# Optimization experiments

Hardware: AMD Instinct MI355X
Metric: run time of the kernel (lower is better)

Reference implementation:

```python
import jax, jax.numpy as jnp
import numpy as np

B, N, M, C1, C2 = 4, 8192, 2048, 128, 256
H1, H2 = 256, 128  # mlp = [C2+C1, 256, 128]
EPS_DIST = 1e-8
EPS_BN = 1e-5
K = 3


def setup_inputs() -> dict:
    key = jax.random.key(0)
    ks = jax.random.split(key, 6)
    return {
        "unknown": jax.random.normal(ks[0], (B, N, 3), dtype=jnp.float32),
        "known": jax.random.normal(ks[1], (B, M, 3), dtype=jnp.float32),
        "unknow_feats": jax.random.normal(ks[2], (B, C1, N), dtype=jnp.float32),
        "known_feats": jax.random.normal(ks[3], (B, C2, M), dtype=jnp.float32),
        "W1": jax.random.normal(ks[4], (H1, C1 + C2), dtype=jnp.float32) * 0.05,
        "g1": jnp.ones((H1,), jnp.float32),
        "b1": jnp.zeros((H1,), jnp.float32),
        "W2": jax.random.normal(ks[5], (H2, H1), dtype=jnp.float32) * 0.05,
        "g2": jnp.ones((H2,), jnp.float32),
        "b2": jnp.zeros((H2,), jnp.float32),
    }


def _bn_relu(x, g, b):
    # training-mode BatchNorm over (batch, spatial) axes for (B, C, N) tensor
    mean = jnp.mean(x, axis=(0, 2), keepdims=True)
    var = jnp.var(x, axis=(0, 2), keepdims=True)
    y = (x - mean) * jax.lax.rsqrt(var + EPS_BN) * g[None, :, None] + b[None, :, None]
    return jax.nn.relu(y)


def reference(unknown, known, unknow_feats, known_feats, W1, g1, b1, W2, g2, b2):
    # 3-NN: squared euclidean distances (B, N, M) via expansion (avoids B,N,M,3 temp)
    d2 = (
        jnp.sum(unknown * unknown, axis=-1)[:, :, None]
        + jnp.sum(known * known, axis=-1)[:, None, :]
        - 2.0 * jnp.einsum("bnc,bmc->bnm", unknown, known)
    )
    neg_d, idx = jax.lax.top_k(-d2, K)  # smallest-K squared dists
    dist = -neg_d  # (B, N, K), squared distances (pytorch3d knn_points convention)
    recip = 1.0 / (dist + EPS_DIST)
    weight = recip / jnp.sum(recip, axis=2, keepdims=True)  # (B, N, K)

    kf = jnp.swapaxes(known_feats, 1, 2)  # (B, M, C2)
    grouped = jax.vmap(lambda f, i: f[i])(kf, idx)  # (B, N, K, C2)
    interp = jnp.einsum("bnkc,bnk->bcn", grouped, weight)  # (B, C2, N)

    x = jnp.concatenate([interp, unknow_feats], axis=1)  # (B, C2+C1, N)
    x = _bn_relu(jnp.einsum("oc,bcn->bon", W1, x), g1, b1)
    x = _bn_relu(jnp.einsum("oc,bcn->bon", W2, x), g2, b2)
    return x  # (B, H2, N)
```

## Files before the change

kernel.cpp:

```cpp
#include <hip/hip_runtime.h>
#include <hip/hip_bf16.h>
#include <cstdint>
#include <cstddef>

typedef unsigned short u16;
typedef __attribute__((ext_vector_type(8))) short bf16x8;
typedef __attribute__((ext_vector_type(4))) float f32x4;

constexpr int Bn = 4;
constexpr int Nq = 8192;
constexpr int Mk = 2048;
constexpr int C1c = 128;
constexpr int C2c = 256;
constexpr int H1c = 256;
constexpr int H2c = 128;

__device__ __forceinline__ float bf2f(u16 u) {
    union { uint32_t i; float f; } v;
    v.i = (uint32_t)u << 16;
    return v.f;
}
__device__ __forceinline__ u16 f2bf(float f) {
    const uint32_t x = __float_as_uint(f);
    return (u16)((x + 0x7FFFu + ((x >> 16) & 1u)) >> 16);
}
__device__ __forceinline__ uint32_t cvtpk(float lo, float hi) {
    uint32_t r;
    asm("v_cvt_pk_bf16_f32 %0, %1, %2" : "=v"(r) : "v"(lo), "v"(hi));
    return r;
}

__global__ __launch_bounds__(256) void knn_prep_kernel(
    const float* __restrict__ W1, const float* __restrict__ W2,
    u16* __restrict__ W1b, u16* __restrict__ W2b,
    const float* __restrict__ KF, u16* __restrict__ Ptb,
    const float* __restrict__ UF, u16* __restrict__ UFt,
    const float* __restrict__ unknown, const float* __restrict__ known,
    int* __restrict__ idx_out, float* __restrict__ w_out)
{
    __shared__ __align__(16) char smem[32768];
    const int bid = blockIdx.x;
    const int t = threadIdx.x;

    if (bid < 1024) {
        float4* kp = (float4*)smem;
        const int b = bid >> 8;
        const int n0 = (bid & 255) * 32;

        const float* kb = known + (size_t)b * Mk * 3;
        for (int i = t; i < Mk; i += 256) {
            const float x = kb[i * 3 + 0], y = kb[i * 3 + 1], z = kb[i * 3 + 2];
            kp[i] = make_float4(x, y, z, fmaf(x, x, fmaf(y, y, z * z)));
        }
        __syncthreads();

        const int q = n0 + (t >> 3);
        const int s = t & 7;
        const float* u = unknown + ((size_t)b * Nq + q) * 3;
        const float ux = u[0], uy = u[1], uz = u[2];
        const float nux = -2.0f * ux, nuy = -2.0f * uy, nuz = -2.0f * uz;
        const float uu = fmaf(ux, ux, fmaf(uy, uy, uz * uz));

        float d0 = 1e30f, d1 = 1e30f, d2 = 1e30f;
        int i0 = 0, i1 = 0, i2 = 0;

        auto ins = [&](float d, int i) {
            const bool c0 = d < d0, c1 = d < d1, c2 = d < d2;
            const float nd0 = fminf(d0, d);
            const float nd1 = __builtin_amdgcn_fmed3f(d0, d, d1);
            const float nd2 = __builtin_amdgcn_fmed3f(d1, d, d2);
            i2 = c1 ? i1 : (c2 ? i : i2);
            i1 = c0 ? i0 : (c1 ? i : i1);
            i0 = c0 ? i : i0;
            d0 = nd0; d1 = nd1; d2 = nd2;
        };

        #pragma unroll 8
        for (int it = 0; it < Mk / 8; ++it) {
            const int m = it * 8 + s;
            const float4 p = kp[m];
            const float d = fmaf(nux, p.x, fmaf(nuy, p.y, fmaf(nuz, p.z, p.w)));
            ins(d, m);
        }
        #pragma unroll
        for (int off = 1; off <= 4; off <<= 1) {
            const float e0 = __shfl_xor(d0, off), e1 = __shfl_xor(d1, off), e2 = __shfl_xor(d2, off);
            const int j0 = __shfl_xor(i0, off), j1 = __shfl_xor(i1, off), j2 = __shfl_xor(i2, off);
            ins(e0, j0);
            ins(e1, j1);
            ins(e2, j2);
        }
        if (s == 0) {
            const float f0 = d0 + uu, f1 = d1 + uu, f2 = d2 + uu;
            const float r0 = 1.0f / (f0 + 1e-8f);
            const float r1 = 1.0f / (f1 + 1e-8f);
            const float r2 = 1.0f / (f2 + 1e-8f);
            const float inv = 1.0f / (r0 + r1 + r2);
            const size_t base = ((size_t)b * Nq + q) * 3;
            idx_out[base + 0] = i0;
            idx_out[base + 1] = i1;
            idx_out[base + 2] = i2;
            w_out[base + 0] = r0 * inv;
            w_out[base + 1] = r1 * inv;
            w_out[base + 2] = r2 * inv;
        }
    } else if (bid < 1152) {
        const int cb = bid - 1024;
        const float* X = (cb < 96) ? W1 : W2;
        u16* Y = (cb < 96) ? W1b : W2b;
        const int i = ((cb < 96) ? cb : (cb - 96)) * 256 + t;
        const float4 v = *(const float4*)&X[(size_t)i * 4];
        ushort4 o;
        o.x = f2bf(v.x); o.y = f2bf(v.y); o.z = f2bf(v.z); o.w = f2bf(v.w);
        *(ushort4*)&Y[(size_t)i * 4] = o;
    } else if (bid < 1664) {
        u16* As = (u16*)smem;
        u16* Bs = (u16*)(smem + 5120);
        const int f = bid - 1152;
        const int b = f >> 7;
        const int rem = f & 127;
        const int m0 = (rem >> 2) * 64;
        const int h0 = (rem & 3) * 64;
        const float* KFb = KF + (size_t)b * C2c * Mk;
        const int l = t & 63, wv = t >> 6;
        const int wr = wv >> 1, wc = wv & 1;

        f32x4 acc[2][2];
        const f32x4 z = {0.0f, 0.0f, 0.0f, 0.0f};
        acc[0][0] = z; acc[0][1] = z; acc[1][0] = z; acc[1][1] = z;

        const int cA = t >> 3;
        const int mcA = (t & 7) * 8;
        const int hB = t >> 2;
        const int khB = (t & 3) * 8;

        for (int kt = 0; kt < 8; ++kt) {
            const int kc = kt * 32;
            {
                const float* src = &KFb[(size_t)(kc + cA) * Mk + m0 + mcA];
                const float4 v0 = *(const float4*)&src[0];
                const float4 v1 = *(const float4*)&src[4];
                As[(mcA + 0) * 40 + cA] = f2bf(v0.x);
                As[(mcA + 1) * 40 + cA] = f2bf(v0.y);
                As[(mcA + 2) * 40 + cA] = f2bf(v0.z);
                As[(mcA + 3) * 40 + cA] = f2bf(v0.w);
                As[(mcA + 4) * 40 + cA] = f2bf(v1.x);
                As[(mcA + 5) * 40 + cA] = f2bf(v1.y);
                As[(mcA + 6) * 40 + cA] = f2bf(v1.z);
                As[(mcA + 7) * 40 + cA] = f2bf(v1.w);
            }
            {
                const float* src = &W1[(size_t)(h0 + hB) * 384 + kc + khB];
                const float4 v0 = *(const float4*)&src[0];
                const float4 v1 = *(const float4*)&src[4];
                u16 o[8] = {f2bf(v0.x), f2bf(v0.y), f2bf(v0.z), f2bf(v0.w),
                            f2bf(v1.x), f2bf(v1.y), f2bf(v1.z), f2bf(v1.w)};
                *(uint4*)&Bs[hB * 40 + khB] = *(const uint4*)o;
            }
            __syncthreads();
            bf16x8 af[2], bf[2];
            #pragma unroll
            for (int ff = 0; ff < 2; ++ff) {
                af[ff] = *(const bf16x8*)&As[(wr * 32 + ff * 16 + (l & 15)) * 40 + (l >> 4) * 8];
                bf[ff] = *(const bf16x8*)&Bs[(wc * 32 + ff * 16 + (l & 15)) * 40 + (l >> 4) * 8];
            }
            #pragma unroll
            for (int i = 0; i < 2; ++i)
                #pragma unroll
                for (int j = 0; j < 2; ++j)
                    acc[i][j] = __builtin_amdgcn_mfma_f32_16x16x32_bf16(af[i], bf[j], acc[i][j], 0, 0, 0);
            __syncthreads();
        }

        u16* Pb = Ptb + (size_t)b * Mk * 256;
        const int cb = l & 15, rg = (l >> 4) * 4;
        #pragma unroll
        for (int i = 0; i < 2; ++i) {
            #pragma unroll
            for (int r = 0; r < 4; ++r) {
                const int row = m0 + wr * 32 + i * 16 + rg + r;
                #pragma unroll
                for (int j = 0; j < 2; ++j)
                    Pb[(size_t)row * 256 + h0 + wc * 32 + j * 16 + cb] = f2bf(acc[i][j][r]);
            }
        }
    } else {
        const int f = bid - 1664;
        const int b = f >> 8, rem = f & 255;
        const int m0 = (rem >> 1) * 64, c0 = (rem & 1) * 64;
        const float* X = UF + (size_t)b * C1c * Nq;
        u16* Y = UFt + (size_t)b * Nq * C1c;
        float (*T)[65] = (float(*)[65])smem;
        const int m4 = (t & 15) * 4, cr = t >> 4;
        #pragma unroll
        for (int i = 0; i < 4; ++i) {
            const float4 v = *(const float4*)&X[(size_t)(c0 + cr + i * 16) * Nq + m0 + m4];
            T[cr + i * 16][m4 + 0] = v.x;
            T[cr + i * 16][m4 + 1] = v.y;
            T[cr + i * 16][m4 + 2] = v.z;
            T[cr + i * 16][m4 + 3] = v.w;
        }
        __syncthreads();
        const int c4 = (t & 15) * 4, mr = t >> 4;
        #pragma unroll
        for (int i = 0; i < 4; ++i) {
            const int m = mr + i * 16;
            ushort4 o;
            o.x = f2bf(T[c4 + 0][m]);
            o.y = f2bf(T[c4 + 1][m]);
            o.z = f2bf(T[c4 + 2][m]);
            o.w = f2bf(T[c4 + 3][m]);
            *(ushort4*)&Y[(size_t)(m0 + m) * C1c + c0 + c4] = o;
        }
    }
}

__global__ __launch_bounds__(256) void mfma_gemm2(
    const u16* __restrict__ A,
    const u16* __restrict__ Bt,
    u16* __restrict__ Cout,
    const u16* __restrict__ Ptb,
    const int* __restrict__ idx, const float* __restrict__ wgt,
    float* __restrict__ partS, float* __restrict__ partQ)
{
    __shared__ u16 As[4096];
    __shared__ u16 Bs[4096];
    __shared__ float sS[2][128], sQ[2][128];

    const int b = blockIdx.z;
    const int m0 = blockIdx.x * 128, n0 = blockIdx.y * 128;
    const int t = threadIdx.x;
    const int l = t & 63, wv = t >> 6;
    const int wr = wv >> 1, wc = wv & 1;

    const u16* Ab = A + (size_t)b * Nq * C1c;
    const int rA0 = t >> 2, rA1 = (t + 256) >> 2;
    const int ko = (t & 3) * 8;

    f32x4 acc[4][4];
    const f32x4 z = {0.0f, 0.0f, 0.0f, 0.0f};
    #pragma unroll
    for (int i = 0; i < 4; ++i)
        #pragma unroll
        for (int j = 0; j < 4; ++j) acc[i][j] = z;

    uint4 a0 = *(const uint4*)&Ab[(size_t)(m0 + rA0) * C1c + ko];
    uint4 a1 = *(const uint4*)&Ab[(size_t)(m0 + rA1) * C1c + ko];
    uint4 b0 = *(const uint4*)&Bt[(size_t)(n0 + rA0) * 384 + ko];
    uint4 b1 = *(const uint4*)&Bt[(size_t)(n0 + rA1) * 384 + ko];

    for (int kt = 0; kt < C1c / 32; ++kt) {
        *(uint4*)&As[t * 8] = a0;
        *(uint4*)&As[(t + 256) * 8] = a1;
        *(uint4*)&Bs[t * 8] = b0;
        *(uint4*)&Bs[(t + 256) * 8] = b1;
        __syncthreads();
        if (kt + 1 < C1c / 32) {
            const int k0 = (kt + 1) * 32;
            a0 = *(const uint4*)&Ab[(size_t)(m0 + rA0) * C1c + k0 + ko];
            a1 = *(const uint4*)&Ab[(size_t)(m0 + rA1) * C1c + k0 + ko];
            b0 = *(const uint4*)&Bt[(size_t)(n0 + rA0) * 384 + k0 + ko];
            b1 = *(const uint4*)&Bt[(size_t)(n0 + rA1) * 384 + k0 + ko];
        }
        bf16x8 af[4], bf[4];
        #pragma unroll
        for (int f = 0; f < 4; ++f) {
            af[f] = *(const bf16x8*)&As[(wr * 64 + f * 16 + (l & 15)) * 32 + (l >> 4) * 8];
            bf[f] = *(const bf16x8*)&Bs[(wc * 64 + f * 16 + (l & 15)) * 32 + (l >> 4) * 8];
        }
        #pragma unroll
        for (int i = 0; i < 4; ++i)
            #pragma unroll
            for (int j = 0; j < 4; ++j)
                acc[i][j] = __builtin_amdgcn_mfma_f32_16x16x32_bf16(af[i], bf[j], acc[i][j], 0, 0, 0);
        __syncthreads();
    }

    const int cb = l & 15;
    const int rg = (l >> 4) * 4;
    float sj[4] = {0, 0, 0, 0}, qj[4] = {0, 0, 0, 0};
    #pragma unroll
    for (int i = 0; i < 4; ++i) {
        #pragma unroll
        for (int r = 0; r < 4; ++r) {
            const int R = m0 + wr * 64 + i * 16 + rg + r;
            const size_t ib = ((size_t)b * Nq + R) * 3;
            const int j0 = idx[ib], j1 = idx[ib + 1], j2 = idx[ib + 2];
            const float w0 = wgt[ib], w1 = wgt[ib + 1], w2 = wgt[ib + 2];
            const u16* Pb = Ptb + (size_t)b * Mk * 256;
            const u16* P0 = Pb + (size_t)j0 * 256;
            const u16* P1 = Pb + (size_t)j1 * 256;
            const u16* P2 = Pb + (size_t)j2 * 256;
            #pragma unroll
            for (int j = 0; j < 4; ++j) {
                const int Cc = n0 + wc * 64 + j * 16 + cb;
                float v = acc[i][j][r];
                v += w0 * bf2f(P0[Cc]) + w1 * bf2f(P1[Cc]) + w2 * bf2f(P2[Cc]);
                Cout[(size_t)b * Nq * 256 + (size_t)R * 256 + Cc] = f2bf(v);
                sj[j] += v;
                qj[j] += v * v;
            }
        }
    }

    #pragma unroll
    for (int j = 0; j < 4; ++j) {
        float s = sj[j], q = qj[j];
        s += __shfl_xor(s, 16); s += __shfl_xor(s, 32);
        q += __shfl_xor(q, 16); q += __shfl_xor(q, 32);
        if (l < 16) {
            sS[wr][wc * 64 + j * 16 + l] = s;
            sQ[wr][wc * 64 + j * 16 + l] = q;
        }
    }
    __syncthreads();
    if (t < 128) {
        const float S = sS[0][t] + sS[1][t];
        const float Q = sQ[0][t] + sQ[1][t];
        const int pblk = blockIdx.z * gridDim.x + blockIdx.x;
        partS[(size_t)pblk * 256 + blockIdx.y * 128 + t] = S;
        partQ[(size_t)pblk * 256 + blockIdx.y * 128 + t] = Q;
    }
}

__global__ __launch_bounds__(1024) void bn_finalize(
    const float* __restrict__ pS, const float* __restrict__ pQ,
    const float* __restrict__ g, const float* __restrict__ beta,
    float* __restrict__ scale, float* __restrict__ bias,
    int C, int np, float cnt)
{
    __shared__ float rs[1024], rq[1024];
    const int t = threadIdx.x;
    const int c = t & (C - 1);
    const int sl = t / C;
    const int nsl = 1024 / C;
    float s = 0.0f, q = 0.0f;
    for (int i = sl; i < np; i += nsl) {
        s += pS[(size_t)i * C + c];
        q += pQ[(size_t)i * C + c];
    }
    rs[t] = s;
    rq[t] = q;
    __syncthreads();
    if (t < C) {
        for (int k = 1; k < nsl; ++k) {
            s += rs[t + k * C];
            q += rq[t + k * C];
        }
        const float mean = s / cnt;
        const float var = q / cnt - mean * mean;
        const float r = rsqrtf(var + 1e-5f);
        const float sc = g[t] * r;
        scale[t] = sc;
        bias[t] = beta[t] - mean * sc;
    }
}

__device__ __forceinline__ uint4 bnx(uint4 x, const float* scs, const float* bis, int k) {
    const u16* p = (const u16*)&x;
    const float4 s0 = *(const float4*)&scs[k];
    const float4 s1 = *(const float4*)&scs[k + 4];
    const float4 b0 = *(const float4*)&bis[k];
    const float4 b1 = *(const float4*)&bis[k + 4];
    const float* sa = (const float*)&s0;
    const float* sb = (const float*)&s1;
    const float* ba = (const float*)&b0;
    const float* bb = (const float*)&b1;
    uint4 o;
    uint32_t* po = (uint32_t*)&o;
    #pragma unroll
    for (int w2 = 0; w2 < 2; ++w2) {
        const float a0 = fmaxf(0.0f, fmaf(bf2f(p[2 * w2 + 0]), sa[2 * w2 + 0], ba[2 * w2 + 0]));
        const float a1 = fmaxf(0.0f, fmaf(bf2f(p[2 * w2 + 1]), sa[2 * w2 + 1], ba[2 * w2 + 1]));
        po[w2] = cvtpk(a0, a1);
    }
    #pragma unroll
    for (int w2 = 0; w2 < 2; ++w2) {
        const float a0 = fmaxf(0.0f, fmaf(bf2f(p[4 + 2 * w2 + 0]), sb[2 * w2 + 0], bb[2 * w2 + 0]));
        const float a1 = fmaxf(0.0f, fmaf(bf2f(p[4 + 2 * w2 + 1]), sb[2 * w2 + 1], bb[2 * w2 + 1]));
        po[2 + w2] = cvtpk(a0, a1);
    }
    return o;
}

__global__ __launch_bounds__(256) void mfma_gemm3(
    const u16* __restrict__ W2b,
    const u16* __restrict__ Y,
    float* __restrict__ out,
    const float* __restrict__ bn_s, const float* __restrict__ bn_b,
    float* __restrict__ partS, float* __restrict__ partQ)
{
    __shared__ u16 As[2048];
    __shared__ u16 Bs[4096];
    __shared__ float scs[256], bis[256];
    __shared__ float sS[2][64], sQ[2][64];

    const int b = blockIdx.z;
    const int m0 = blockIdx.x * 64;
    const int n0 = blockIdx.y * 128;
    const int t = threadIdx.x;
    const int l = t & 63, wv = t >> 6;
    const int wr = wv >> 1, wc = wv & 1;

    scs[t] = bn_s[t];
    bis[t] = bn_b[t];

    const u16* Yb = Y + (size_t)b * Nq * 256;
    const int rA = t >> 2;
    const int rB1 = (t + 256) >> 2;
    const int ko = (t & 3) * 8;

    f32x4 acc[2][4];
    const f32x4 z = {0.0f, 0.0f, 0.0f, 0.0f};
    #pragma unroll
    for (int i = 0; i < 2; ++i)
        #pragma unroll
        for (int j = 0; j < 4; ++j) acc[i][j] = z;

    uint4 a0 = *(const uint4*)&W2b[(size_t)(m0 + rA) * 256 + ko];
    uint4 b0 = *(const uint4*)&Yb[(size_t)(n0 + rA) * 256 + ko];
    uint4 b1 = *(const uint4*)&Yb[(size_t)(n0 + rB1) * 256 + ko];
    __syncthreads();

    for (int kt = 0; kt < 8; ++kt) {
        const int k = kt * 32 + ko;
        *(uint4*)&As[t * 8] = a0;
        *(uint4*)&Bs[t * 8] = bnx(b0, scs, bis, k);
        *(uint4*)&Bs[(t + 256) * 8] = bnx(b1, scs, bis, k);
        __syncthreads();
        if (kt + 1 < 8) {
            const int k0 = (kt + 1) * 32;
            a0 = *(const uint4*)&W2b[(size_t)(m0 + rA) * 256 + k0 + ko];
            b0 = *(const uint4*)&Yb[(size_t)(n0 + rA) * 256 + k0 + ko];
            b1 = *(const uint4*)&Yb[(size_t)(n0 + rB1) * 256 + k0 + ko];
        }
        bf16x8 af[2], bf[4];
        #pragma unroll
        for (int f = 0; f < 2; ++f)
            af[f] = *(const bf16x8*)&As[(wr * 32 + f * 16 + (l & 15)) * 32 + (l >> 4) * 8];
        #pragma unroll
        for (int f = 0; f < 4; ++f)
            bf[f] = *(const bf16x8*)&Bs[(wc * 64 + f * 16 + (l & 15)) * 32 + (l >> 4) * 8];
        #pragma unroll
        for (int i = 0; i < 2; ++i)
            #pragma unroll
            for (int j = 0; j < 4; ++j)
                acc[i][j] = __builtin_amdgcn_mfma_f32_16x16x32_bf16(af[i], bf[j], acc[i][j], 0, 0, 0);
        __syncthreads();
    }

    const int cb = l & 15;
    const int rg = (l >> 4) * 4;
    float* ob = out + (size_t)b * H2c * Nq;
    #pragma unroll
    for (int i = 0; i < 2; ++i) {
        #pragma unroll
        for (int r = 0; r < 4; ++r) {
            const int Rl = wr * 32 + i * 16 + rg + r;
            #pragma unroll
            for (int j = 0; j < 4; ++j) {
                const int Cc = n0 + wc * 64 + j * 16 + cb;
                ob[(size_t)(m0 + Rl) * Nq + Cc] = acc[i][j][r];
            }
            float s = acc[i][0][r] + acc[i][1][r] + acc[i][2][r] + acc[i][3][r];
            float q = acc[i][0][r] * acc[i][0][r] + acc[i][1][r] * acc[i][1][r] +
                      acc[i][2][r] * acc[i][2][r] + acc[i][3][r] * acc[i][3][r];
            s += __shfl_xor(s, 1); s += __shfl_xor(s, 2);
            s += __shfl_xor(s, 4); s += __shfl_xor(s, 8);
            q += __shfl_xor(q, 1); q += __shfl_xor(q, 2);
            q += __shfl_xor(q, 4); q += __shfl_xor(q, 8);
            if ((l & 15) == 0) {
                sS[wc][Rl] = s;
                sQ[wc][Rl] = q;
            }
        }
    }
    __syncthreads();
    if (t < 64) {
        const float S = sS[0][t] + sS[1][t];
        const float Q = sQ[0][t] + sQ[1][t];
        const int p = blockIdx.z * gridDim.y + blockIdx.y;
        partS[(size_t)p * 128 + m0 + t] = S;
        partQ[(size_t)p * 128 + m0 + t] = Q;
    }
}

__global__ __launch_bounds__(256) void bn2_apply_kernel(
    float* __restrict__ Y,
    const float* __restrict__ pS, const float* __restrict__ pQ,
    const float* __restrict__ g, const float* __restrict__ beta)
{
    __shared__ float rs[256], rq[256];
    const int t = threadIdx.x;
    const size_t base = (size_t)blockIdx.x * 1024;
    const int c = (int)((base / Nq) % H2c);

    rs[t] = pS[(size_t)t * 128 + c];
    rq[t] = pQ[(size_t)t * 128 + c];
    __syncthreads();
    for (int off = 128; off > 0; off >>= 1) {
        if (t < off) {
            rs[t] += rs[t + off];
            rq[t] += rq[t + off];
        }
        __syncthreads();
    }
    if (t == 0) {
        const float cnt = (float)(Bn * Nq);
        const float mean = rs[0] / cnt;
        const float var = rq[0] / cnt - mean * mean;
        const float r = rsqrtf(var + 1e-5f);
        const float sc = g[c] * r;
        rs[0] = sc;
        rq[0] = beta[c] - mean * sc;
    }
    __syncthreads();
    const float sc = rs[0], bi = rq[0];
    float4 v = *(float4*)&Y[base + t * 4];
    v.x = fmaxf(0.0f, fmaf(v.x, sc, bi));
    v.y = fmaxf(0.0f, fmaf(v.y, sc, bi));
    v.z = fmaxf(0.0f, fmaf(v.z, sc, bi));
    v.w = fmaxf(0.0f, fmaf(v.w, sc, bi));
    *(float4*)&Y[base + t * 4] = v;
}

extern "C" void kernel_launch(void* const* d_in, const int* in_sizes, int n_in,
                              void* d_out, int out_size, void* d_ws, size_t ws_size,
                              hipStream_t stream) {
    const float* unknown = (const float*)d_in[0];
    const float* known = (const float*)d_in[1];
    const float* unknow_feats = (const float*)d_in[2];
    const float* known_feats = (const float*)d_in[3];
    const float* W1 = (const float*)d_in[4];
    const float* g1 = (const float*)d_in[5];
    const float* b1 = (const float*)d_in[6];
    const float* W2 = (const float*)d_in[7];
    const float* g2 = (const float*)d_in[8];
    const float* b2 = (const float*)d_in[9];
    float* out = (float*)d_out;

    char* w = (char*)d_ws;
    u16* UFt = (u16*)w; w += (size_t)Bn * Nq * C1c * 2;
    u16* W1b = (u16*)w; w += (size_t)H1c * 384 * 2;
    u16* W2b = (u16*)w; w += (size_t)H2c * H1c * 2;
    u16* Ptb = (u16*)w; w += (size_t)Bn * Mk * H1c * 2;
    u16* y1b = (u16*)w; w += (size_t)Bn * Nq * H1c * 2;
    int* idx = (int*)w; w += (size_t)Bn * Nq * 3 * 4;
    float* wgt = (float*)w; w += (size_t)Bn * Nq * 3 * 4;
    float* pS1 = (float*)w; w += (size_t)256 * 256 * 4;
    float* pQ1 = (float*)w; w += (size_t)256 * 256 * 4;
    float* pS2 = (float*)w; w += (size_t)256 * 128 * 4;
    float* pQ2 = (float*)w; w += (size_t)256 * 128 * 4;
    float* scale1 = (float*)w; w += 1024;
    float* bias1 = (float*)w; w += 1024;

    knn_prep_kernel<<<2688, 256, 0, stream>>>(W1, W2, W1b, W2b,
                                              known_feats, Ptb, unknow_feats, UFt,
                                              unknown, known, idx, wgt);

    mfma_gemm2<<<dim3(Nq / 128, H1c / 128, Bn), 256, 0, stream>>>(
        UFt, W1b + C2c, y1b, Ptb, idx, wgt, pS1, pQ1);

    bn_finalize<<<1, 1024, 0, stream>>>(pS1, pQ1, g1, b1, scale1, bias1,
                                        H1c, 256, (float)(Bn * Nq));

    mfma_gemm3<<<dim3(2, Nq / 128, Bn), 256, 0, stream>>>(
        W2b, y1b, out, scale1, bias1, pS2, pQ2);

    bn2_apply_kernel<<<(Bn * H2c * Nq) / 1024, 256, 0, stream>>>(out, pS2, pQ2, g2, b2);
}
```

Baseline: 103.4 us.

## Stage GEMM1 epilogue through LDS for vectorized gather and stores; multi-block BN finalize

The GEMM1 epilogue now writes accumulator tiles to shared memory in 32-row chunks, then each thread handles 8 contiguous channels per row. It gathers the three neighbor feature rows with 16-byte loads and writes bf16 output with 16-byte stores, replacing scattered 2-byte gathers and stores. The BN1 finalize moves from one 1024-thread block to 16 blocks of 256 threads, one per 16-channel group. The epilogue gains extra syncthreads and LDS round trips in exchange for coalesced global access.

```diff
diff --git a/kernel.cpp b/kernel.cpp
--- a/kernel.cpp
+++ b/kernel.cpp
@@ -223,9 +223,11 @@
     const int* __restrict__ idx, const float* __restrict__ wgt,
     float* __restrict__ partS, float* __restrict__ partQ)
 {
-    __shared__ u16 As[4096];
-    __shared__ u16 Bs[4096];
-    __shared__ float sS[2][128], sQ[2][128];
+    __shared__ __align__(16) char smem[16384];
+    __shared__ float redS[4][128], redQ[4][128];
+    u16* As = (u16*)smem;
+    u16* Bs = (u16*)(smem + 8192);
+    float (*Ytmp)[128] = (float(*)[128])smem;
 
     const int b = blockIdx.z;
     const int m0 = blockIdx.x * 128, n0 = blockIdx.y * 128;
@@ -278,81 +280,119 @@
 
     const int cb = l & 15;
     const int rg = (l >> 4) * 4;
-    float sj[4] = {0, 0, 0, 0}, qj[4] = {0, 0, 0, 0};
-    #pragma unroll
-    for (int i = 0; i < 4; ++i) {
-        #pragma unroll
-        for (int r = 0; r < 4; ++r) {
-            const int R = m0 + wr * 64 + i * 16 + rg + r;
+    const int colblk = t & 15;
+    const int rowblk = t >> 4;
+    float s8[8] = {0, 0, 0, 0, 0, 0, 0, 0}, q8[8] = {0, 0, 0, 0, 0, 0, 0, 0};
+    const u16* Pb = Ptb + (size_t)b * Mk * 256;
+
+    for (int q = 0; q < 4; ++q) {
+        __syncthreads();
+        if (wr == (q >> 1)) {
+            #pragma unroll
+            for (int ii = 0; ii < 2; ++ii) {
+                const int i = (q & 1) * 2 + ii;
+                #pragma unroll
+                for (int r = 0; r < 4; ++r) {
+                    const int Rq = ii * 16 + rg + r;
+                    #pragma unroll
+                    for (int j = 0; j < 4; ++j)
+                        Ytmp[Rq][wc * 64 + j * 16 + cb] = acc[i][j][r];
+                }
+            }
+        }
+        __syncthreads();
+        #pragma unroll
+        for (int rr = 0; rr < 2; ++rr) {
+            const int Rq = rowblk * 2 + rr;
+            const int R = m0 + q * 32 + Rq;
             const size_t ib = ((size_t)b * Nq + R) * 3;
             const int j0 = idx[ib], j1 = idx[ib + 1], j2 = idx[ib + 2];
             const float w0 = wgt[ib], w1 = wgt[ib + 1], w2 = wgt[ib + 2];
-            const u16* Pb = Ptb + (size_t)b * Mk * 256;
-            const u16* P0 = Pb + (size_t)j0 * 256;
-            const u16* P1 = Pb + (size_t)j1 * 256;
-            const u16* P2 = Pb + (size_t)j2 * 256;
-            #pragma unroll
-            for (int j = 0; j < 4; ++j) {
-                const int Cc = n0 + wc * 64 + j * 16 + cb;
-                float v = acc[i][j][r];
-                v += w0 * bf2f(P0[Cc]) + w1 * bf2f(P1[Cc]) + w2 * bf2f(P2[Cc]);
-                Cout[(size_t)b * Nq * 256 + (size_t)R * 256 + Cc] = f2bf(v);
-                sj[j] += v;
-                qj[j] += v * v;
-            }
+            const int c8 = colblk * 8;
+            const int Cc0 = n0 + c8;
+            const float* yrow = &Ytmp[Rq][c8];
+            const float4 y0 = *(const float4*)&yrow[0];
+            const float4 y1v = *(const float4*)&yrow[4];
+            const uint4 p0 = *(const uint4*)&Pb[(size_t)j0 * 256 + Cc0];
+            const uint4 p1 = *(const uint4*)&Pb[(size_t)j1 * 256 + Cc0];
+            const uint4 p2 = *(const uint4*)&Pb[(size_t)j2 * 256 + Cc0];
+            const u16* pp0 = (const u16*)&p0;
+            const u16* pp1 = (const u16*)&p1;
+            const u16* pp2 = (const u16*)&p2;
+            const float* ya = (const float*)&y0;
+            const float* yb = (const float*)&y1v;
+            float v[8];
+            #pragma unroll
+            for (int c = 0; c < 8; ++c) {
+                const float a = (c < 4) ? ya[c] : yb[c - 4];
+                const float vv = a + w0 * bf2f(pp0[c]) + w1 * bf2f(pp1[c]) + w2 * bf2f(pp2[c]);
+                v[c] = vv;
+                s8[c] += vv;
+                q8[c] += vv * vv;
+            }
+            uint4 o;
+            uint32_t* po = (uint32_t*)&o;
+            po[0] = cvtpk(v[0], v[1]);
+            po[1] = cvtpk(v[2], v[3]);
+            po[2] = cvtpk(v[4], v[5]);
+            po[3] = cvtpk(v[6], v[7]);
+            *(uint4*)&Cout[(size_t)b * Nq * 256 + (size_t)R * 256 + Cc0] = o;
         }
     }
 
     #pragma unroll
-    for (int j = 0; j < 4; ++j) {
-        float s = sj[j], q = qj[j];
-        s += __shfl_xor(s, 16); s += __shfl_xor(s, 32);
-        q += __shfl_xor(q, 16); q += __shfl_xor(q, 32);
-        if (l < 16) {
-            sS[wr][wc * 64 + j * 16 + l] = s;
-            sQ[wr][wc * 64 + j * 16 + l] = q;
+    for (int c = 0; c < 8; ++c) {
+        s8[c] += __shfl_xor(s8[c], 16);
+        s8[c] += __shfl_xor(s8[c], 32);
+        q8[c] += __shfl_xor(q8[c], 16);
+        q8[c] += __shfl_xor(q8[c], 32);
+    }
+    if (l < 16) {
+        #pragma unroll
+        for (int c = 0; c < 8; ++c) {
+            redS[wv][l * 8 + c] = s8[c];
+            redQ[wv][l * 8 + c] = q8[c];
         }
     }
     __syncthreads();
     if (t < 128) {
-        const float S = sS[0][t] + sS[1][t];
-        const float Q = sQ[0][t] + sQ[1][t];
+        const float S = redS[0][t] + redS[1][t] + redS[2][t] + redS[3][t];
+        const float Q = redQ[0][t] + redQ[1][t] + redQ[2][t] + redQ[3][t];
         const int pblk = blockIdx.z * gridDim.x + blockIdx.x;
         partS[(size_t)pblk * 256 + blockIdx.y * 128 + t] = S;
         partQ[(size_t)pblk * 256 + blockIdx.y * 128 + t] = Q;
     }
 }
 
-__global__ __launch_bounds__(1024) void bn_finalize(
+__global__ __launch_bounds__(256) void bn1_finalize_mb(
     const float* __restrict__ pS, const float* __restrict__ pQ,
     const float* __restrict__ g, const float* __restrict__ beta,
-    float* __restrict__ scale, float* __restrict__ bias,
-    int C, int np, float cnt)
+    float* __restrict__ scale, float* __restrict__ bias)
 {
-    __shared__ float rs[1024], rq[1024];
-    const int t = threadIdx.x;
-    const int c = t & (C - 1);
-    const int sl = t / C;
-    const int nsl = 1024 / C;
+    __shared__ float rs[256], rq[256];
+    const int cc = threadIdx.x & 15;
+    const int sl = threadIdx.x >> 4;
+    const int ch = blockIdx.x * 16 + cc;
     float s = 0.0f, q = 0.0f;
-    for (int i = sl; i < np; i += nsl) {
-        s += pS[(size_t)i * C + c];
-        q += pQ[(size_t)i * C + c];
-    }
-    rs[t] = s;
-    rq[t] = q;
+    for (int i = sl; i < 256; i += 16) {
+        s += pS[(size_t)i * 256 + ch];
+        q += pQ[(size_t)i * 256 + ch];
+    }
+    rs[threadIdx.x] = s;
+    rq[threadIdx.x] = q;
     __syncthreads();
-    if (t < C) {
-        for (int k = 1; k < nsl; ++k) {
-            s += rs[t + k * C];
-            q += rq[t + k * C];
-        }
+    if (sl == 0) {
+        for (int k = 1; k < 16; ++k) {
+            s += rs[k * 16 + cc];
+            q += rq[k * 16 + cc];
+        }
+        const float cnt = (float)(Bn * Nq);
         const float mean = s / cnt;
         const float var = q / cnt - mean * mean;
-        const float r = rsqrtf(var + 1e-5f);
-        const float sc = g[t] * r;
-        scale[t] = sc;
-        bias[t] = beta[t] - mean * sc;
+        const float rv = rsqrtf(var + 1e-5f);
+        const float sc = g[ch] * rv;
+        scale[ch] = sc;
+        bias[ch] = beta[ch] - mean * sc;
     }
 }
 
@@ -561,8 +601,7 @@
     mfma_gemm2<<<dim3(Nq / 128, H1c / 128, Bn), 256, 0, stream>>>(
         UFt, W1b + C2c, y1b, Ptb, idx, wgt, pS1, pQ1);
 
-    bn_finalize<<<1, 1024, 0, stream>>>(pS1, pQ1, g1, b1, scale1, bias1,
-                                        H1c, 256, (float)(Bn * Nq));
+    bn1_finalize_mb<<<16, 256, 0, stream>>>(pS1, pQ1, g1, b1, scale1, bias1);
 
     mfma_gemm3<<<dim3(2, Nq / 128, Bn), 256, 0, stream>>>(
         W2b, y1b, out, scale1, bias1, pS2, pQ2);
```

Measured after the change: 92.68 us. -10.4%, faster.
